# Kernel optimization log

Measured on AMD Instinct MI355X. Metric: run time of the kernel, lower is better.

Reference implementation:

```python
import math
import jax, jax.numpy as jnp
import numpy as np

GROUPS = 8
EPS = 1e-5


def setup_inputs() -> dict:
    key = jax.random.key(0)
    ks = jax.random.split(key, 4)
    B, C, H, W = 4, 128, 64, 64
    x = jax.random.normal(ks[0], (B, C, H, W), dtype=jnp.float32)
    norm_w = jnp.ones((C,), dtype=jnp.float32)
    norm_b = jnp.zeros((C,), dtype=jnp.float32)
    qkv_w = jax.random.normal(ks[1], (3 * C, C), dtype=jnp.float32) * 0.02
    qkv_b = jnp.zeros((3 * C,), dtype=jnp.float32)
    proj_w = jax.random.normal(ks[2], (C, C), dtype=jnp.float32) * 0.02
    proj_b = jnp.zeros((C,), dtype=jnp.float32)
    return {"x": x, "norm_w": norm_w, "norm_b": norm_b,
            "qkv_w": qkv_w, "qkv_b": qkv_b,
            "proj_w": proj_w, "proj_b": proj_b}


def reference(x, norm_w, norm_b, qkv_w, qkv_b, proj_w, proj_b):
    B, C, H, W = x.shape
    N = H * W
    # GroupNorm over (C/G, H, W) per group
    xr = x.reshape(B, GROUPS, C // GROUPS, N)
    mean = xr.mean(axis=(2, 3), keepdims=True)
    var = xr.var(axis=(2, 3), keepdims=True)
    h = ((xr - mean) * jax.lax.rsqrt(var + EPS)).reshape(B, C, N)
    h = h * norm_w[None, :, None] + norm_b[None, :, None]
    # 1x1 conv QKV == per-pixel linear: [B, 3C, N]
    qkv = jnp.einsum('oc,bcn->bon', qkv_w, h) + qkv_b[None, :, None]
    q, k, v = jnp.split(qkv, 3, axis=1)  # each [B, C, N]
    scale = 1.0 / math.sqrt(C)
    attn = jax.nn.softmax(jnp.einsum('bci,bcj->bij', q, k) * scale, axis=-1)  # [B,N,N]
    out = jnp.einsum('bij,bcj->bci', attn, v)  # [B, C, N]
    proj = jnp.einsum('oc,bcn->bon', proj_w, out) + proj_b[None, :, None]
    return x + proj.reshape(B, C, H, W)
```

## Files before the change

kernel.cpp:

```cpp
#include <hip/hip_runtime.h>

typedef float  f32x4   __attribute__((ext_vector_type(4)));
typedef float  f32x16  __attribute__((ext_vector_type(16)));
typedef short  bf16x8  __attribute__((ext_vector_type(8)));
typedef unsigned short u16;

constexpr int B_ = 4;
constexpr int C_ = 128;
constexpr int N_ = 4096;
constexpr int G_ = 8;
constexpr int CperG = 16;
constexpr float EPS_ = 1e-5f;
constexpr float SCALE_ = 0.08838834764831845f;

__device__ inline u16 f2bf(float f) {
    union { float f; unsigned u; } v; v.f = f;
    unsigned r = v.u + 0x7fffu + ((v.u >> 16) & 1u);
    return (u16)(r >> 16);
}
__device__ inline unsigned pk2(float a, float b) {
    return (unsigned)f2bf(a) | ((unsigned)f2bf(b) << 16);
}

__global__ __launch_bounds__(256) void prep_kernel(const float* __restrict__ x,
                                                   const float* __restrict__ qw,
                                                   const float* __restrict__ pw,
                                                   float* __restrict__ stats2,
                                                   u16* __restrict__ qwbf,
                                                   u16* __restrict__ pwbf) {
    int blk = blockIdx.x;
    if (blk < 256) {
        __shared__ float rs[4], rss[4];
        int bg = blk >> 3, chunk = blk & 7;
        const float4* xp = (const float4*)(x + (size_t)bg * (CperG * N_)) + chunk * 2048;
        float s = 0.f, ss = 0.f;
        for (int i = threadIdx.x; i < 2048; i += 256) {
            float4 v = xp[i];
            s  += v.x + v.y + v.z + v.w;
            ss += v.x*v.x + v.y*v.y + v.z*v.z + v.w*v.w;
        }
        #pragma unroll
        for (int off = 32; off > 0; off >>= 1) {
            s  += __shfl_down(s, off);
            ss += __shfl_down(ss, off);
        }
        int wv = threadIdx.x >> 6, ln = threadIdx.x & 63;
        if (ln == 0) { rs[wv] = s; rss[wv] = ss; }
        __syncthreads();
        if (threadIdx.x == 0) {
            stats2[blk*2]     = rs[0] + rs[1] + rs[2] + rs[3];
            stats2[blk*2 + 1] = rss[0] + rss[1] + rss[2] + rss[3];
        }
    } else {
        int fidx = ((blk - 256) * 256 + threadIdx.x) * 4;
        float4 v;
        u16* dst;
        if (fidx < 3*C_*C_) { v = *(const float4*)(qw + fidx); dst = qwbf + fidx; }
        else { int j = fidx - 3*C_*C_; v = *(const float4*)(pw + j); dst = pwbf + j; }
        ushort4 o;
        o.x = f2bf(v.x); o.y = f2bf(v.y); o.z = f2bf(v.z); o.w = f2bf(v.w);
        *(ushort4*)dst = o;
    }
}

constexpr int HS = 136;

__global__ __launch_bounds__(256, 2) void qkv_kernel(const float* __restrict__ x,
                                                     const float* __restrict__ stats2,
                                                     const float* __restrict__ nw,
                                                     const float* __restrict__ nb,
                                                     const u16* __restrict__ qwbf,
                                                     const float* __restrict__ qb,
                                                     u16* __restrict__ Qt,
                                                     u16* __restrict__ Ksw,
                                                     u16* __restrict__ Vsw,
                                                     float* __restrict__ qn2,
                                                     int* __restrict__ kmaxI) {
    int n0 = (blockIdx.x & 63) * 64;
    int b  = blockIdx.x >> 6;
    __shared__ u16 hs[64 * HS];
    __shared__ u16 Wl[64 * HS];
    __shared__ float gmean[8], grstd[8];
    int t = threadIdx.x;
    const float invM = 1.f / (float)(CperG * N_);
    if (t < 8) {
        const float* sp = stats2 + (size_t)(b*G_ + t)*16;
        float S = 0.f, SS = 0.f;
        #pragma unroll
        for (int k2 = 0; k2 < 8; ++k2) { S += sp[k2*2]; SS += sp[k2*2 + 1]; }
        float mean = S * invM;
        gmean[t] = mean;
        grstd[t] = rsqrtf(SS * invM - mean*mean + EPS_);
    }
    __syncthreads();
    #pragma unroll
    for (int r = 0; r < 8; ++r) {
        int idx = t + (r << 8);
        int c = idx >> 4, n4 = idx & 15;
        int g = c >> 4;
        float wgt = nw[c] * grstd[g];
        float bia = nb[c] - gmean[g] * wgt;
        float4 xv = *(const float4*)(x + ((size_t)(b*C_ + c))*N_ + n0 + n4*4);
        int base = (n4*4) * HS + c;
        hs[base         ] = f2bf(xv.x*wgt + bia);
        hs[base +     HS] = f2bf(xv.y*wgt + bia);
        hs[base + 2 * HS] = f2bf(xv.z*wgt + bia);
        hs[base + 3 * HS] = f2bf(xv.w*wgt + bia);
    }
    __syncthreads();
    int w = t >> 6, lane = t & 63, lo = lane & 15, hi = lane >> 4;
    bf16x8 hf[4];
    #pragma unroll
    for (int ch = 0; ch < 4; ++ch)
        hf[ch] = *(const bf16x8*)(hs + (16*w + lo)*HS + 32*ch + 8*hi);

    int Tb = (n0 >> 5) + (w >> 1);
    float nq = 0.f, nk = 0.f;
    for (int ck = 0; ck < 6; ++ck) {
        {
            int r = t >> 2, p = t & 3;
            const u16* src = qwbf + (size_t)(ck*64 + r)*C_ + p*32;
            u16* dst = Wl + r*HS + p*32;
            #pragma unroll
            for (int k2 = 0; k2 < 4; ++k2)
                *(uint4*)(dst + 8*k2) = *(const uint4*)(src + 8*k2);
        }
        __syncthreads();
        #pragma unroll
        for (int ot = 0; ot < 4; ++ot) {
            int o16 = ck*64 + ot*16;
            bf16x8 wf[4];
            #pragma unroll
            for (int ch = 0; ch < 4; ++ch)
                wf[ch] = *(const bf16x8*)(Wl + (ot*16 + lo)*HS + 32*ch + 8*hi);
            if (o16 < 2*C_) {
                f32x4 acc = (f32x4){0.f, 0.f, 0.f, 0.f};
                #pragma unroll
                for (int ch = 0; ch < 4; ++ch)
                    acc = __builtin_amdgcn_mfma_f32_16x16x32_bf16(wf[ch], hf[ch], acc, 0, 0, 0);
                float4 bv = *(const float4*)(qb + o16 + 4*hi);
                int n = n0 + 16*w + lo;
                ushort4 o4;
                if (o16 < C_) {
                    float q0 = (acc[0] + bv.x) * SCALE_;
                    float q1 = (acc[1] + bv.y) * SCALE_;
                    float q2 = (acc[2] + bv.z) * SCALE_;
                    float q3 = (acc[3] + bv.w) * SCALE_;
                    nq += (q0*q0 + q1*q1) + (q2*q2 + q3*q3);
                    o4.x = f2bf(q0); o4.y = f2bf(q1); o4.z = f2bf(q2); o4.w = f2bf(q3);
                    *(ushort4*)(Qt + ((size_t)b*N_ + n)*C_ + o16 + 4*hi) = o4;
                } else {
                    float k0 = acc[0] + bv.x, k1 = acc[1] + bv.y;
                    float k2 = acc[2] + bv.z, k3 = acc[3] + bv.w;
                    nk += (k0*k0 + k1*k1) + (k2*k2 + k3*k3);
                    o4.x = f2bf(k0); o4.y = f2bf(k1); o4.z = f2bf(k2); o4.w = f2bf(k3);
                    int cc = (o16 - C_) >> 4;
                    int lp = (16*(w & 1) + lo) + 32*(hi >> 1);
                    size_t fb = ((size_t)(b*128 + Tb)*8 + cc)*512;
                    *(ushort4*)(Ksw + fb + lp*8 + 4*(hi & 1)) = o4;
                }
            } else {
                f32x4 acc = (f32x4){0.f, 0.f, 0.f, 0.f};
                #pragma unroll
                for (int ch = 0; ch < 4; ++ch)
                    acc = __builtin_amdgcn_mfma_f32_16x16x32_bf16(hf[ch], wf[ch], acc, 0, 0, 0);
                float bia = qb[o16 + lo];
                ushort4 o4;
                o4.x = f2bf(acc[0] + bia);
                o4.y = f2bf(acc[1] + bia);
                o4.z = f2bf(acc[2] + bia);
                o4.w = f2bf(acc[3] + bia);
                int m  = (o16 - 2*C_) >> 4;
                int ct = m >> 1;
                int lp = (16*(m & 1) + lo) + 32*(hi & 1);
                size_t fb = (((size_t)(b*4 + ct)*128 + Tb)*2 + (w & 1))*512;
                *(ushort4*)(Vsw + fb + lp*8 + 4*(hi >> 1)) = o4;
            }
        }
        __syncthreads();
    }
    nq += __shfl_xor(nq, 16); nq += __shfl_xor(nq, 32);
    nk += __shfl_xor(nk, 16); nk += __shfl_xor(nk, 32);
    if (lane < 16) qn2[(size_t)b*N_ + n0 + 16*w + lo] = nq;
    #pragma unroll
    for (int off = 1; off < 16; off <<= 1)
        nk = fmaxf(nk, __shfl_xor(nk, off));
    if (lane == 0) atomicMax(&kmaxI[b], __float_as_int(nk));
}

__global__ __launch_bounds__(512, 2) void attn_kernel(const u16* __restrict__ Qt,
                                                      const u16* __restrict__ Ksw,
                                                      const u16* __restrict__ Vsw,
                                                      const float* __restrict__ qn2,
                                                      const int* __restrict__ kmaxI,
                                                      const u16* __restrict__ pwbf,
                                                      const float* __restrict__ pb,
                                                      const float* __restrict__ x,
                                                      float* __restrict__ out) {
    int lb = blockIdx.x;
    int b  = lb & 3;
    int i0 = 64 * (lb >> 2);
    int t = threadIdx.x;
    int w = t >> 6, lane = t & 63;
    int l31 = lane & 31, h = lane >> 5;
    int qt = w >> 2, ks = w & 3;

    __shared__ float Ob[64 * 132];
    __shared__ float lW[8][32];

    float kmax = sqrtf(__int_as_float(kmaxI[b]));
    float mq = sqrtf(qn2[(size_t)b*N_ + i0 + 32*qt + l31]) * kmax * 1.02f + 1e-6f;

    const u16* Qb = Qt + (size_t)b*N_*C_;
    bf16x8 qf[8];
    #pragma unroll
    for (int cc = 0; cc < 8; ++cc)
        qf[cc] = *(const bf16x8*)(Qb + (size_t)(i0 + 32*qt + l31)*C_ + 16*cc + 8*h);

    f32x16 acc[4];
    #pragma unroll
    for (int ct = 0; ct < 4; ++ct)
        #pragma unroll
        for (int r = 0; r < 16; ++r) acc[ct][r] = 0.f;
    float psum = 0.f;

    const u16* Kbase = Ksw + ((size_t)(b*128 + ks*32)*8)*512;
    bf16x8 kf[8], kn[8];
    #pragma unroll
    for (int cc = 0; cc < 8; ++cc)
        kf[cc] = *(const bf16x8*)(Kbase + cc*512 + lane*8);

    for (int it = 0; it < 32; ++it) {
        f32x16 s;
        #pragma unroll
        for (int r = 0; r < 16; ++r) s[r] = 0.f;
        #pragma unroll
        for (int cc = 0; cc < 8; ++cc)
            s = __builtin_amdgcn_mfma_f32_32x32x16_bf16(kf[cc], qf[cc], s, 0, 0, 0);
        {
            const u16* Kn = Kbase + ((size_t)(((it + 1) & 31))*8)*512;
            #pragma unroll
            for (int cc = 0; cc < 8; ++cc)
                kn[cc] = *(const bf16x8*)(Kn + cc*512 + lane*8);
        }
        int T = ks*32 + it;
        bf16x8 v1[4], v2[4];
        #pragma unroll
        for (int ct = 0; ct < 4; ++ct) {
            const u16* vb = Vsw + (((size_t)(b*4 + ct)*128 + T)*2)*512;
            v1[ct] = *(const bf16x8*)(vb + lane*8);
            v2[ct] = *(const bf16x8*)(vb + 512 + lane*8);
        }
        float p[16];
        #pragma unroll
        for (int r = 0; r < 16; ++r) {
            p[r] = __expf(s[r] - mq);
            psum += p[r];
        }
        union { bf16x8 v; unsigned u[4]; } pf1, pf2;
        pf1.u[0] = pk2(p[0],  p[1]);  pf1.u[1] = pk2(p[2],  p[3]);
        pf1.u[2] = pk2(p[4],  p[5]);  pf1.u[3] = pk2(p[6],  p[7]);
        pf2.u[0] = pk2(p[8],  p[9]);  pf2.u[1] = pk2(p[10], p[11]);
        pf2.u[2] = pk2(p[12], p[13]); pf2.u[3] = pk2(p[14], p[15]);
        #pragma unroll
        for (int ct = 0; ct < 4; ++ct) {
            acc[ct] = __builtin_amdgcn_mfma_f32_32x32x16_bf16(v1[ct], pf1.v, acc[ct], 0, 0, 0);
            acc[ct] = __builtin_amdgcn_mfma_f32_32x32x16_bf16(v2[ct], pf2.v, acc[ct], 0, 0, 0);
        }
        #pragma unroll
        for (int cc = 0; cc < 8; ++cc) kf[cc] = kn[cc];
    }

    psum += __shfl_xor(psum, 32);
    if (lane < 32) lW[w][l31] = psum;
    for (int i = 0; i < 4; ++i) {
        if (ks == i) {
            int q = 32*qt + l31;
            #pragma unroll
            for (int ct = 0; ct < 4; ++ct)
                #pragma unroll
                for (int qd = 0; qd < 4; ++qd) {
                    int c = 32*ct + 8*qd + 4*h;
                    float4 vv;
                    vv.x = acc[ct][4*qd + 0];
                    vv.y = acc[ct][4*qd + 1];
                    vv.z = acc[ct][4*qd + 2];
                    vv.w = acc[ct][4*qd + 3];
                    if (i == 0) {
                        *(float4*)(Ob + q*132 + c) = vv;
                    } else {
                        float4 o = *(const float4*)(Ob + q*132 + c);
                        o.x += vv.x; o.y += vv.y; o.z += vv.z; o.w += vv.w;
                        *(float4*)(Ob + q*132 + c) = o;
                    }
                }
        }
        __syncthreads();
    }
    int lo = lane & 15, hi = lane >> 4;
    int qtile = w >> 1, os = w & 1;
    int q = 16*qtile + lo;
    int qg = 4*(q >> 5), qc = q & 31;
    float linv = 1.f / (lW[qg][qc] + lW[qg+1][qc] + lW[qg+2][qc] + lW[qg+3][qc]);
    bf16x8 aa[4];
    #pragma unroll
    for (int ch = 0; ch < 4; ++ch) {
        float4 ua = *(const float4*)(Ob + q*132 + 32*ch + 8*hi);
        float4 ub = *(const float4*)(Ob + q*132 + 32*ch + 8*hi + 4);
        union { bf16x8 hh; unsigned u[4]; } pkd;
        pkd.u[0] = pk2(ua.x*linv, ua.y*linv);
        pkd.u[1] = pk2(ua.z*linv, ua.w*linv);
        pkd.u[2] = pk2(ub.x*linv, ub.y*linv);
        pkd.u[3] = pk2(ub.z*linv, ub.w*linv);
        aa[ch] = pkd.hh;
    }
    #pragma unroll
    for (int ot = 0; ot < 4; ++ot) {
        int ob = 64*os + 16*ot;
        f32x4 pr = (f32x4){0.f, 0.f, 0.f, 0.f};
        #pragma unroll
        for (int ch = 0; ch < 4; ++ch) {
            bf16x8 bw = *(const bf16x8*)(pwbf + (size_t)(ob + lo)*C_ + 32*ch + 8*hi);
            pr = __builtin_amdgcn_mfma_f32_16x16x32_bf16(aa[ch], bw, pr, 0, 0, 0);
        }
        int o = ob + lo;
        float pbv = pb[o];
        size_t base = ((size_t)(b*C_ + o))*N_ + i0 + 16*qtile + 4*hi;
        float4 xr = *(const float4*)(x + base);
        float4 res;
        res.x = xr.x + pr[0] + pbv;
        res.y = xr.y + pr[1] + pbv;
        res.z = xr.z + pr[2] + pbv;
        res.w = xr.w + pr[3] + pbv;
        *(float4*)(out + base) = res;
    }
}

extern "C" void kernel_launch(void* const* d_in, const int* in_sizes, int n_in,
                              void* d_out, int out_size, void* d_ws, size_t ws_size,
                              hipStream_t stream) {
    const float* x  = (const float*)d_in[0];
    const float* nw = (const float*)d_in[1];
    const float* nb = (const float*)d_in[2];
    const float* qw = (const float*)d_in[3];
    const float* qb = (const float*)d_in[4];
    const float* pw = (const float*)d_in[5];
    const float* pb = (const float*)d_in[6];
    float* out = (float*)d_out;

    char* p = (char*)d_ws;
    float* stats2 = (float*)p;                 p += 2048;
    float* qn2    = (float*)p;                 p += (size_t)B_*N_*4;
    int*   kmaxI  = (int*)p;                   p += 256;
    u16*   qwbf   = (u16*)p;                   p += (size_t)3*C_*C_*2;
    u16*   pwbf   = (u16*)p;                   p += (size_t)C_*C_*2;
    u16*   Qt     = (u16*)p;                   p += (size_t)B_*N_*C_*2;
    u16*   Ksw    = (u16*)p;                   p += (size_t)B_*N_*C_*2;
    u16*   Vsw    = (u16*)p;

    prep_kernel<<<dim3(320), 256, 0, stream>>>(x, qw, pw, stats2, qwbf, pwbf);
    qkv_kernel<<<dim3(256), 256, 0, stream>>>(x, stats2, nw, nb, qwbf, qb,
                                              Qt, Ksw, Vsw, qn2, kmaxI);
    attn_kernel<<<dim3(256), 512, 0, stream>>>(Qt, Ksw, Vsw, qn2, kmaxI,
                                               pwbf, pb, x, out);
}
```

Baseline: 152.8 us.

## Fuse prep, QKV and attention into one cooperative kernel with grid syncs

Replaces the three kernel launches with one cooperative kernel of 256 blocks by 512 threads. Phases are separated by grid.sync: stats and weight conversion first, then QKV projection, then attention. The QKV phase now uses 8 waves that split the output chunks across two wave groups, and norms are combined through shared memory. This removes launch gaps and inter-kernel drain, at the cost of grid-wide barriers, larger shared memory per block and lower occupancy in the QKV phase. The kmaxI reset is not visible in the shown code.

```diff
diff --git a/kernel.cpp b/kernel.cpp
--- a/kernel.cpp
+++ b/kernel.cpp
@@ -1,4 +1,7 @@
 #include <hip/hip_runtime.h>
+#include <hip/hip_cooperative_groups.h>
+
+namespace cg = cooperative_groups;
 
 typedef float  f32x4   __attribute__((ext_vector_type(4)));
 typedef float  f32x16  __attribute__((ext_vector_type(16)));
@@ -12,6 +15,7 @@
 constexpr int CperG = 16;
 constexpr float EPS_ = 1e-5f;
 constexpr float SCALE_ = 0.08838834764831845f;
+constexpr int HS = 136;
 
 __device__ inline u16 f2bf(float f) {
     union { float f; unsigned u; } v; v.f = f;
@@ -22,20 +26,43 @@
     return (unsigned)f2bf(a) | ((unsigned)f2bf(b) << 16);
 }
 
-__global__ __launch_bounds__(256) void prep_kernel(const float* __restrict__ x,
-                                                   const float* __restrict__ qw,
-                                                   const float* __restrict__ pw,
-                                                   float* __restrict__ stats2,
-                                                   u16* __restrict__ qwbf,
-                                                   u16* __restrict__ pwbf) {
+__global__ __launch_bounds__(512, 2) void fused_kernel(const float* __restrict__ x,
+                                                       const float* __restrict__ nw,
+                                                       const float* __restrict__ nb,
+                                                       const float* __restrict__ qw,
+                                                       const float* __restrict__ qb,
+                                                       const float* __restrict__ pw,
+                                                       const float* __restrict__ pb,
+                                                       float* __restrict__ stats2,
+                                                       float* __restrict__ qn2,
+                                                       int* __restrict__ kmaxI,
+                                                       u16* __restrict__ qwbf,
+                                                       u16* __restrict__ pwbf,
+                                                       u16* __restrict__ Qt,
+                                                       u16* __restrict__ Ksw,
+                                                       u16* __restrict__ Vsw,
+                                                       float* __restrict__ out) {
+    cg::grid_group grid = cg::this_grid();
+
+    __shared__ u16 hs[64 * HS];
+    __shared__ u16 Wl[128 * HS];
+    __shared__ float Ob[64 * 132];
+    __shared__ float lW[8][32];
+    __shared__ float rs[8], rss[8];
+    __shared__ float gmean[8], grstd[8];
+    __shared__ float nqS[2][64], nkS[2][64];
+
     int blk = blockIdx.x;
-    if (blk < 256) {
-        __shared__ float rs[4], rss[4];
+    int t = threadIdx.x;
+    int w = t >> 6, lane = t & 63, lo = lane & 15, hi = lane >> 4;
+
+    {
         int bg = blk >> 3, chunk = blk & 7;
         const float4* xp = (const float4*)(x + (size_t)bg * (CperG * N_)) + chunk * 2048;
         float s = 0.f, ss = 0.f;
-        for (int i = threadIdx.x; i < 2048; i += 256) {
-            float4 v = xp[i];
+        #pragma unroll
+        for (int r = 0; r < 4; ++r) {
+            float4 v = xp[t + (r << 9)];
             s  += v.x + v.y + v.z + v.w;
             ss += v.x*v.x + v.y*v.y + v.z*v.z + v.w*v.w;
         }
@@ -44,295 +71,280 @@
             s  += __shfl_down(s, off);
             ss += __shfl_down(ss, off);
         }
-        int wv = threadIdx.x >> 6, ln = threadIdx.x & 63;
-        if (ln == 0) { rs[wv] = s; rss[wv] = ss; }
-        __syncthreads();
-        if (threadIdx.x == 0) {
-            stats2[blk*2]     = rs[0] + rs[1] + rs[2] + rs[3];
-            stats2[blk*2 + 1] = rss[0] + rss[1] + rss[2] + rss[3];
-        }
-    } else {
-        int fidx = ((blk - 256) * 256 + threadIdx.x) * 4;
-        float4 v;
-        u16* dst;
-        if (fidx < 3*C_*C_) { v = *(const float4*)(qw + fidx); dst = qwbf + fidx; }
-        else { int j = fidx - 3*C_*C_; v = *(const float4*)(pw + j); dst = pwbf + j; }
-        ushort4 o;
-        o.x = f2bf(v.x); o.y = f2bf(v.y); o.z = f2bf(v.z); o.w = f2bf(v.w);
-        *(ushort4*)dst = o;
+        if (lane == 0) { rs[w] = s; rss[w] = ss; }
+        if (t < 64) {
+            int fidx = (blk*64 + t) * 4;
+            float4 v;
+            u16* dst;
+            if (fidx < 3*C_*C_) { v = *(const float4*)(qw + fidx); dst = qwbf + fidx; }
+            else { int j = fidx - 3*C_*C_; v = *(const float4*)(pw + j); dst = pwbf + j; }
+            ushort4 o;
+            o.x = f2bf(v.x); o.y = f2bf(v.y); o.z = f2bf(v.z); o.w = f2bf(v.w);
+            *(ushort4*)dst = o;
+        }
+        __syncthreads();
+        if (t == 0) {
+            float S = 0.f, SS = 0.f;
+            #pragma unroll
+            for (int i = 0; i < 8; ++i) { S += rs[i]; SS += rss[i]; }
+            stats2[blk*2]     = S;
+            stats2[blk*2 + 1] = SS;
+        }
     }
-}
-
-constexpr int HS = 136;
-
-__global__ __launch_bounds__(256, 2) void qkv_kernel(const float* __restrict__ x,
-                                                     const float* __restrict__ stats2,
-                                                     const float* __restrict__ nw,
-                                                     const float* __restrict__ nb,
-                                                     const u16* __restrict__ qwbf,
-                                                     const float* __restrict__ qb,
-                                                     u16* __restrict__ Qt,
-                                                     u16* __restrict__ Ksw,
-                                                     u16* __restrict__ Vsw,
-                                                     float* __restrict__ qn2,
-                                                     int* __restrict__ kmaxI) {
-    int n0 = (blockIdx.x & 63) * 64;
-    int b  = blockIdx.x >> 6;
-    __shared__ u16 hs[64 * HS];
-    __shared__ u16 Wl[64 * HS];
-    __shared__ float gmean[8], grstd[8];
-    int t = threadIdx.x;
-    const float invM = 1.f / (float)(CperG * N_);
-    if (t < 8) {
-        const float* sp = stats2 + (size_t)(b*G_ + t)*16;
-        float S = 0.f, SS = 0.f;
-        #pragma unroll
-        for (int k2 = 0; k2 < 8; ++k2) { S += sp[k2*2]; SS += sp[k2*2 + 1]; }
-        float mean = S * invM;
-        gmean[t] = mean;
-        grstd[t] = rsqrtf(SS * invM - mean*mean + EPS_);
-    }
-    __syncthreads();
-    #pragma unroll
-    for (int r = 0; r < 8; ++r) {
-        int idx = t + (r << 8);
-        int c = idx >> 4, n4 = idx & 15;
-        int g = c >> 4;
-        float wgt = nw[c] * grstd[g];
-        float bia = nb[c] - gmean[g] * wgt;
-        float4 xv = *(const float4*)(x + ((size_t)(b*C_ + c))*N_ + n0 + n4*4);
-        int base = (n4*4) * HS + c;
-        hs[base         ] = f2bf(xv.x*wgt + bia);
-        hs[base +     HS] = f2bf(xv.y*wgt + bia);
-        hs[base + 2 * HS] = f2bf(xv.z*wgt + bia);
-        hs[base + 3 * HS] = f2bf(xv.w*wgt + bia);
-    }
-    __syncthreads();
-    int w = t >> 6, lane = t & 63, lo = lane & 15, hi = lane >> 4;
-    bf16x8 hf[4];
-    #pragma unroll
-    for (int ch = 0; ch < 4; ++ch)
-        hf[ch] = *(const bf16x8*)(hs + (16*w + lo)*HS + 32*ch + 8*hi);
-
-    int Tb = (n0 >> 5) + (w >> 1);
-    float nq = 0.f, nk = 0.f;
-    for (int ck = 0; ck < 6; ++ck) {
-        {
-            int r = t >> 2, p = t & 3;
-            const u16* src = qwbf + (size_t)(ck*64 + r)*C_ + p*32;
-            u16* dst = Wl + r*HS + p*32;
-            #pragma unroll
-            for (int k2 = 0; k2 < 4; ++k2)
-                *(uint4*)(dst + 8*k2) = *(const uint4*)(src + 8*k2);
-        }
-        __syncthreads();
-        #pragma unroll
-        for (int ot = 0; ot < 4; ++ot) {
-            int o16 = ck*64 + ot*16;
-            bf16x8 wf[4];
-            #pragma unroll
-            for (int ch = 0; ch < 4; ++ch)
-                wf[ch] = *(const bf16x8*)(Wl + (ot*16 + lo)*HS + 32*ch + 8*hi);
-            if (o16 < 2*C_) {
-                f32x4 acc = (f32x4){0.f, 0.f, 0.f, 0.f};
+    __threadfence();
+    grid.sync();
+
+    {
+        int n0 = (blk & 63) * 64;
+        int b  = blk >> 6;
+        const float invM = 1.f / (float)(CperG * N_);
+        if (t < 8) {
+            const float* sp = stats2 + (size_t)(b*G_ + t)*16;
+            float S = 0.f, SS = 0.f;
+            #pragma unroll
+            for (int k2 = 0; k2 < 8; ++k2) { S += sp[k2*2]; SS += sp[k2*2 + 1]; }
+            float mean = S * invM;
+            gmean[t] = mean;
+            grstd[t] = rsqrtf(SS * invM - mean*mean + EPS_);
+        }
+        __syncthreads();
+        #pragma unroll
+        for (int r = 0; r < 4; ++r) {
+            int idx = t + (r << 9);
+            int c = idx >> 4, n4 = idx & 15;
+            int g = c >> 4;
+            float wgt = nw[c] * grstd[g];
+            float bia = nb[c] - gmean[g] * wgt;
+            float4 xv = *(const float4*)(x + ((size_t)(b*C_ + c))*N_ + n0 + n4*4);
+            int base = (n4*4) * HS + c;
+            hs[base         ] = f2bf(xv.x*wgt + bia);
+            hs[base +     HS] = f2bf(xv.y*wgt + bia);
+            hs[base + 2 * HS] = f2bf(xv.z*wgt + bia);
+            hs[base + 3 * HS] = f2bf(xv.w*wgt + bia);
+        }
+        __syncthreads();
+        int g2 = w >> 2;
+        int wl = w & 3;
+        bf16x8 hf[4];
+        #pragma unroll
+        for (int ch = 0; ch < 4; ++ch)
+            hf[ch] = *(const bf16x8*)(hs + (16*wl + lo)*HS + 32*ch + 8*hi);
+
+        int Tb = (n0 >> 5) + (wl >> 1);
+        float nq = 0.f, nk = 0.f;
+        for (int ck2 = 0; ck2 < 3; ++ck2) {
+            {
+                int r = t >> 2, p = t & 3;
+                const u16* src = qwbf + (size_t)(ck2*128 + r)*C_ + p*32;
+                u16* dst = Wl + r*HS + p*32;
+                #pragma unroll
+                for (int k2 = 0; k2 < 4; ++k2)
+                    *(uint4*)(dst + 8*k2) = *(const uint4*)(src + 8*k2);
+            }
+            __syncthreads();
+            int chunk = ck2*2 + g2;
+            #pragma unroll
+            for (int ot = 0; ot < 4; ++ot) {
+                int o16 = chunk*64 + ot*16;
+                bf16x8 wf[4];
                 #pragma unroll
                 for (int ch = 0; ch < 4; ++ch)
-                    acc = __builtin_amdgcn_mfma_f32_16x16x32_bf16(wf[ch], hf[ch], acc, 0, 0, 0);
-                float4 bv = *(const float4*)(qb + o16 + 4*hi);
-                int n = n0 + 16*w + lo;
-                ushort4 o4;
-                if (o16 < C_) {
-                    float q0 = (acc[0] + bv.x) * SCALE_;
-                    float q1 = (acc[1] + bv.y) * SCALE_;
-                    float q2 = (acc[2] + bv.z) * SCALE_;
-                    float q3 = (acc[3] + bv.w) * SCALE_;
-                    nq += (q0*q0 + q1*q1) + (q2*q2 + q3*q3);
-                    o4.x = f2bf(q0); o4.y = f2bf(q1); o4.z = f2bf(q2); o4.w = f2bf(q3);
-                    *(ushort4*)(Qt + ((size_t)b*N_ + n)*C_ + o16 + 4*hi) = o4;
+                    wf[ch] = *(const bf16x8*)(Wl + (64*g2 + ot*16 + lo)*HS + 32*ch + 8*hi);
+                if (o16 < 2*C_) {
+                    f32x4 acc = (f32x4){0.f, 0.f, 0.f, 0.f};
+                    #pragma unroll
+                    for (int ch = 0; ch < 4; ++ch)
+                        acc = __builtin_amdgcn_mfma_f32_16x16x32_bf16(wf[ch], hf[ch], acc, 0, 0, 0);
+                    float4 bv = *(const float4*)(qb + o16 + 4*hi);
+                    int n = n0 + 16*wl + lo;
+                    ushort4 o4;
+                    if (o16 < C_) {
+                        float q0 = (acc[0] + bv.x) * SCALE_;
+                        float q1 = (acc[1] + bv.y) * SCALE_;
+                        float q2 = (acc[2] + bv.z) * SCALE_;
+                        float q3 = (acc[3] + bv.w) * SCALE_;
+                        nq += (q0*q0 + q1*q1) + (q2*q2 + q3*q3);
+                        o4.x = f2bf(q0); o4.y = f2bf(q1); o4.z = f2bf(q2); o4.w = f2bf(q3);
+                        *(ushort4*)(Qt + ((size_t)b*N_ + n)*C_ + o16 + 4*hi) = o4;
+                    } else {
+                        float k0 = acc[0] + bv.x, k1 = acc[1] + bv.y;
+                        float k2 = acc[2] + bv.z, k3 = acc[3] + bv.w;
+                        nk += (k0*k0 + k1*k1) + (k2*k2 + k3*k3);
+                        o4.x = f2bf(k0); o4.y = f2bf(k1); o4.z = f2bf(k2); o4.w = f2bf(k3);
+                        int cc = (o16 - C_) >> 4;
+                        int lp = (16*(wl & 1) + lo) + 32*(hi >> 1);
+                        size_t fb = ((size_t)(b*128 + Tb)*8 + cc)*512;
+                        *(ushort4*)(Ksw + fb + lp*8 + 4*(hi & 1)) = o4;
+                    }
                 } else {
-                    float k0 = acc[0] + bv.x, k1 = acc[1] + bv.y;
-                    float k2 = acc[2] + bv.z, k3 = acc[3] + bv.w;
-                    nk += (k0*k0 + k1*k1) + (k2*k2 + k3*k3);
-                    o4.x = f2bf(k0); o4.y = f2bf(k1); o4.z = f2bf(k2); o4.w = f2bf(k3);
-                    int cc = (o16 - C_) >> 4;
-                    int lp = (16*(w & 1) + lo) + 32*(hi >> 1);
-                    size_t fb = ((size_t)(b*128 + Tb)*8 + cc)*512;
-                    *(ushort4*)(Ksw + fb + lp*8 + 4*(hi & 1)) = o4;
+                    f32x4 acc = (f32x4){0.f, 0.f, 0.f, 0.f};
+                    #pragma unroll
+                    for (int ch = 0; ch < 4; ++ch)
+                        acc = __builtin_amdgcn_mfma_f32_16x16x32_bf16(hf[ch], wf[ch], acc, 0, 0, 0);
+                    float bia = qb[o16 + lo];
+                    ushort4 o4;
+                    o4.x = f2bf(acc[0] + bia);
+                    o4.y = f2bf(acc[1] + bia);
+                    o4.z = f2bf(acc[2] + bia);
+                    o4.w = f2bf(acc[3] + bia);
+                    int m  = (o16 - 2*C_) >> 4;
+                    int ct = m >> 1;
+                    int lp = (16*(m & 1) + lo) + 32*(hi & 1);
+                    size_t fb = (((size_t)(b*4 + ct)*128 + Tb)*2 + (wl & 1))*512;
+                    *(ushort4*)(Vsw + fb + lp*8 + 4*(hi >> 1)) = o4;
                 }
-            } else {
-                f32x4 acc = (f32x4){0.f, 0.f, 0.f, 0.f};
+            }
+            __syncthreads();
+        }
+        nq += __shfl_xor(nq, 16); nq += __shfl_xor(nq, 32);
+        nk += __shfl_xor(nk, 16); nk += __shfl_xor(nk, 32);
+        if (lane < 16) { nqS[g2][16*wl + lo] = nq; nkS[g2][16*wl + lo] = nk; }
+        __syncthreads();
+        if (w < 4) {
+            float nqt = nqS[0][16*w + lo] + nqS[1][16*w + lo];
+            float nkt = nkS[0][16*w + lo] + nkS[1][16*w + lo];
+            if (lane < 16) qn2[(size_t)b*N_ + n0 + 16*w + lo] = nqt;
+            #pragma unroll
+            for (int off = 1; off < 16; off <<= 1)
+                nkt = fmaxf(nkt, __shfl_xor(nkt, off));
+            if (lane == 0) atomicMax(&kmaxI[b], __float_as_int(nkt));
+        }
+    }
+    __threadfence();
+    grid.sync();
+
+    {
+        int b  = blk & 3;
+        int i0 = 64 * (blk >> 2);
+        int l31 = lane & 31, h = lane >> 5;
+        int qt = w >> 2, ks = w & 3;
+
+        float kmax = sqrtf(__int_as_float(kmaxI[b]));
+        float mq = sqrtf(qn2[(size_t)b*N_ + i0 + 32*qt + l31]) * kmax * 1.02f + 1e-6f;
+
+        const u16* Qb = Qt + (size_t)b*N_*C_;
+        bf16x8 qf[8];
+        #pragma unroll
+        for (int cc = 0; cc < 8; ++cc)
+            qf[cc] = *(const bf16x8*)(Qb + (size_t)(i0 + 32*qt + l31)*C_ + 16*cc + 8*h);
+
+        f32x16 acc[4];
+        #pragma unroll
+        for (int ct = 0; ct < 4; ++ct)
+            #pragma unroll
+            for (int r = 0; r < 16; ++r) acc[ct][r] = 0.f;
+        float psum = 0.f;
+
+        const u16* Kbase = Ksw + ((size_t)(b*128 + ks*32)*8)*512;
+        bf16x8 kf[8], kn[8];
+        #pragma unroll
+        for (int cc = 0; cc < 8; ++cc)
+            kf[cc] = *(const bf16x8*)(Kbase + cc*512 + lane*8);
+
+        for (int it = 0; it < 32; ++it) {
+            f32x16 s;
+            #pragma unroll
+            for (int r = 0; r < 16; ++r) s[r] = 0.f;
+            #pragma unroll
+            for (int cc = 0; cc < 8; ++cc)
+                s = __builtin_amdgcn_mfma_f32_32x32x16_bf16(kf[cc], qf[cc], s, 0, 0, 0);
+            {
+                const u16* Kn = Kbase + ((size_t)(((it + 1) & 31))*8)*512;
                 #pragma unroll
-                for (int ch = 0; ch < 4; ++ch)
-                    acc = __builtin_amdgcn_mfma_f32_16x16x32_bf16(hf[ch], wf[ch], acc, 0, 0, 0);
-                float bia = qb[o16 + lo];
-                ushort4 o4;
-                o4.x = f2bf(acc[0] + bia);
-                o4.y = f2bf(acc[1] + bia);
-                o4.z = f2bf(acc[2] + bia);
-                o4.w = f2bf(acc[3] + bia);
-                int m  = (o16 - 2*C_) >> 4;
-                int ct = m >> 1;
-                int lp = (16*(m & 1) + lo) + 32*(hi & 1);
-                size_t fb = (((size_t)(b*4 + ct)*128 + Tb)*2 + (w & 1))*512;
-                *(ushort4*)(Vsw + fb + lp*8 + 4*(hi >> 1)) = o4;
-            }
-        }
-        __syncthreads();
-    }
-    nq += __shfl_xor(nq, 16); nq += __shfl_xor(nq, 32);
-    nk += __shfl_xor(nk, 16); nk += __shfl_xor(nk, 32);
-    if (lane < 16) qn2[(size_t)b*N_ + n0 + 16*w + lo] = nq;
-    #pragma unroll
-    for (int off = 1; off < 16; off <<= 1)
-        nk = fmaxf(nk, __shfl_xor(nk, off));
-    if (lane == 0) atomicMax(&kmaxI[b], __float_as_int(nk));
-}
-
-__global__ __launch_bounds__(512, 2) void attn_kernel(const u16* __restrict__ Qt,
-                                                      const u16* __restrict__ Ksw,
-                                                      const u16* __restrict__ Vsw,
-                                                      const float* __restrict__ qn2,
-                                                      const int* __restrict__ kmaxI,
-                                                      const u16* __restrict__ pwbf,
-                                                      const float* __restrict__ pb,
-                                                      const float* __restrict__ x,
-                                                      float* __restrict__ out) {
-    int lb = blockIdx.x;
-    int b  = lb & 3;
-    int i0 = 64 * (lb >> 2);
-    int t = threadIdx.x;
-    int w = t >> 6, lane = t & 63;
-    int l31 = lane & 31, h = lane >> 5;
-    int qt = w >> 2, ks = w & 3;
-
-    __shared__ float Ob[64 * 132];
-    __shared__ float lW[8][32];
-
-    float kmax = sqrtf(__int_as_float(kmaxI[b]));
-    float mq = sqrtf(qn2[(size_t)b*N_ + i0 + 32*qt + l31]) * kmax * 1.02f + 1e-6f;
-
-    const u16* Qb = Qt + (size_t)b*N_*C_;
-    bf16x8 qf[8];
-    #pragma unroll
-    for (int cc = 0; cc < 8; ++cc)
-        qf[cc] = *(const bf16x8*)(Qb + (size_t)(i0 + 32*qt + l31)*C_ + 16*cc + 8*h);
-
-    f32x16 acc[4];
-    #pragma unroll
-    for (int ct = 0; ct < 4; ++ct)
-        #pragma unroll
-        for (int r = 0; r < 16; ++r) acc[ct][r] = 0.f;
-    float psum = 0.f;
-
-    const u16* Kbase = Ksw + ((size_t)(b*128 + ks*32)*8)*512;
-    bf16x8 kf[8], kn[8];
-    #pragma unroll
-    for (int cc = 0; cc < 8; ++cc)
-        kf[cc] = *(const bf16x8*)(Kbase + cc*512 + lane*8);
-
-    for (int it = 0; it < 32; ++it) {
-        f32x16 s;
-        #pragma unroll
-        for (int r = 0; r < 16; ++r) s[r] = 0.f;
-        #pragma unroll
-        for (int cc = 0; cc < 8; ++cc)
-            s = __builtin_amdgcn_mfma_f32_32x32x16_bf16(kf[cc], qf[cc], s, 0, 0, 0);
-        {
-            const u16* Kn = Kbase + ((size_t)(((it + 1) & 31))*8)*512;
-            #pragma unroll
-            for (int cc = 0; cc < 8; ++cc)
-                kn[cc] = *(const bf16x8*)(Kn + cc*512 + lane*8);
-        }
-        int T = ks*32 + it;
-        bf16x8 v1[4], v2[4];
-        #pragma unroll
-        for (int ct = 0; ct < 4; ++ct) {
-            const u16* vb = Vsw + (((size_t)(b*4 + ct)*128 + T)*2)*512;
-            v1[ct] = *(const bf16x8*)(vb + lane*8);
-            v2[ct] = *(const bf16x8*)(vb + 512 + lane*8);
-        }
-        float p[16];
-        #pragma unroll
-        for (int r = 0; r < 16; ++r) {
-            p[r] = __expf(s[r] - mq);
-            psum += p[r];
-        }
-        union { bf16x8 v; unsigned u[4]; } pf1, pf2;
-        pf1.u[0] = pk2(p[0],  p[1]);  pf1.u[1] = pk2(p[2],  p[3]);
-        pf1.u[2] = pk2(p[4],  p[5]);  pf1.u[3] = pk2(p[6],  p[7]);
-        pf2.u[0] = pk2(p[8],  p[9]);  pf2.u[1] = pk2(p[10], p[11]);
-        pf2.u[2] = pk2(p[12], p[13]); pf2.u[3] = pk2(p[14], p[15]);
-        #pragma unroll
-        for (int ct = 0; ct < 4; ++ct) {
-            acc[ct] = __builtin_amdgcn_mfma_f32_32x32x16_bf16(v1[ct], pf1.v, acc[ct], 0, 0, 0);
-            acc[ct] = __builtin_amdgcn_mfma_f32_32x32x16_bf16(v2[ct], pf2.v, acc[ct], 0, 0, 0);
-        }
-        #pragma unroll
-        for (int cc = 0; cc < 8; ++cc) kf[cc] = kn[cc];
-    }
-
-    psum += __shfl_xor(psum, 32);
-    if (lane < 32) lW[w][l31] = psum;
-    for (int i = 0; i < 4; ++i) {
-        if (ks == i) {
-            int q = 32*qt + l31;
-            #pragma unroll
-            for (int ct = 0; ct < 4; ++ct)
+                for (int cc = 0; cc < 8; ++cc)
+                    kn[cc] = *(const bf16x8*)(Kn + cc*512 + lane*8);
+            }
+            int T = ks*32 + it;
+            bf16x8 v1[4], v2[4];
+            #pragma unroll
+            for (int ct = 0; ct < 4; ++ct) {
+                const u16* vb = Vsw + (((size_t)(b*4 + ct)*128 + T)*2)*512;
+                v1[ct] = *(const bf16x8*)(vb + lane*8);
+                v2[ct] = *(const bf16x8*)(vb + 512 + lane*8);
+            }
+            float p[16];
+            #pragma unroll
+            for (int r = 0; r < 16; ++r) {
+                p[r] = __expf(s[r] - mq);
+                psum += p[r];
+            }
+            union { bf16x8 v; unsigned u[4]; } pf1, pf2;
+            pf1.u[0] = pk2(p[0],  p[1]);  pf1.u[1] = pk2(p[2],  p[3]);
+            pf1.u[2] = pk2(p[4],  p[5]);  pf1.u[3] = pk2(p[6],  p[7]);
+            pf2.u[0] = pk2(p[8],  p[9]);  pf2.u[1] = pk2(p[10], p[11]);
+            pf2.u[2] = pk2(p[12], p[13]); pf2.u[3] = pk2(p[14], p[15]);
+            #pragma unroll
+            for (int ct = 0; ct < 4; ++ct) {
+                acc[ct] = __builtin_amdgcn_mfma_f32_32x32x16_bf16(v1[ct], pf1.v, acc[ct], 0, 0, 0);
+                acc[ct] = __builtin_amdgcn_mfma_f32_32x32x16_bf16(v2[ct], pf2.v, acc[ct], 0, 0, 0);
+            }
+            #pragma unroll
+            for (int cc = 0; cc < 8; ++cc) kf[cc] = kn[cc];
+        }
+
+        psum += __shfl_xor(psum, 32);
+        if (lane < 32) lW[w][l31] = psum;
+        __syncthreads();
+        for (int i = 0; i < 4; ++i) {
+            if (ks == i) {
+                int q = 32*qt + l31;
                 #pragma unroll
-                for (int qd = 0; qd < 4; ++qd) {
-                    int c = 32*ct + 8*qd + 4*h;
-                    float4 vv;
-                    vv.x = acc[ct][4*qd + 0];
-                    vv.y = acc[ct][4*qd + 1];
-                    vv.z = acc[ct][4*qd + 2];
-                    vv.w = acc[ct][4*qd + 3];
-                    if (i == 0) {
-                        *(float4*)(Ob + q*132 + c) = vv;
-                    } else {
-                        float4 o = *(const float4*)(Ob + q*132 + c);
-                        o.x += vv.x; o.y += vv.y; o.z += vv.z; o.w += vv.w;
-                        *(float4*)(Ob + q*132 + c) = o;
+                for (int ct = 0; ct < 4; ++ct)
+                    #pragma unroll
+                    for (int qd = 0; qd < 4; ++qd) {
+                        int c = 32*ct + 8*qd + 4*h;
+                        float4 vv;
+                        vv.x = acc[ct][4*qd + 0];
+                        vv.y = acc[ct][4*qd + 1];
+                        vv.z = acc[ct][4*qd + 2];
+                        vv.w = acc[ct][4*qd + 3];
+                        if (i == 0) {
+                            *(float4*)(Ob + q*132 + c) = vv;
+                        } else {
+                            float4 o = *(const float4*)(Ob + q*132 + c);
+                            o.x += vv.x; o.y += vv.y; o.z += vv.z; o.w += vv.w;
+                            *(float4*)(Ob + q*132 + c) = o;
+                        }
                     }
-                }
-        }
-        __syncthreads();
-    }
-    int lo = lane & 15, hi = lane >> 4;
-    int qtile = w >> 1, os = w & 1;
-    int q = 16*qtile + lo;
-    int qg = 4*(q >> 5), qc = q & 31;
-    float linv = 1.f / (lW[qg][qc] + lW[qg+1][qc] + lW[qg+2][qc] + lW[qg+3][qc]);
-    bf16x8 aa[4];
-    #pragma unroll
-    for (int ch = 0; ch < 4; ++ch) {
-        float4 ua = *(const float4*)(Ob + q*132 + 32*ch + 8*hi);
-        float4 ub = *(const float4*)(Ob + q*132 + 32*ch + 8*hi + 4);
-        union { bf16x8 hh; unsigned u[4]; } pkd;
-        pkd.u[0] = pk2(ua.x*linv, ua.y*linv);
-        pkd.u[1] = pk2(ua.z*linv, ua.w*linv);
-        pkd.u[2] = pk2(ub.x*linv, ub.y*linv);
-        pkd.u[3] = pk2(ub.z*linv, ub.w*linv);
-        aa[ch] = pkd.hh;
-    }
-    #pragma unroll
-    for (int ot = 0; ot < 4; ++ot) {
-        int ob = 64*os + 16*ot;
-        f32x4 pr = (f32x4){0.f, 0.f, 0.f, 0.f};
+            }
+            __syncthreads();
+        }
+        int qtile = w >> 1, os = w & 1;
+        int q = 16*qtile + lo;
+        int qg = 4*(q >> 5), qc = q & 31;
+        float linv = 1.f / (lW[qg][qc] + lW[qg+1][qc] + lW[qg+2][qc] + lW[qg+3][qc]);
+        bf16x8 aa[4];
         #pragma unroll
         for (int ch = 0; ch < 4; ++ch) {
-            bf16x8 bw = *(const bf16x8*)(pwbf + (size_t)(ob + lo)*C_ + 32*ch + 8*hi);
-            pr = __builtin_amdgcn_mfma_f32_16x16x32_bf16(aa[ch], bw, pr, 0, 0, 0);
-        }
-        int o = ob + lo;
-        float pbv = pb[o];
-        size_t base = ((size_t)(b*C_ + o))*N_ + i0 + 16*qtile + 4*hi;
-        float4 xr = *(const float4*)(x + base);
-        float4 res;
-        res.x = xr.x + pr[0] + pbv;
-        res.y = xr.y + pr[1] + pbv;
-        res.z = xr.z + pr[2] + pbv;
-        res.w = xr.w + pr[3] + pbv;
-        *(float4*)(out + base) = res;
+            float4 ua = *(const float4*)(Ob + q*132 + 32*ch + 8*hi);
+            float4 ub = *(const float4*)(Ob + q*132 + 32*ch + 8*hi + 4);
+            union { bf16x8 hh; unsigned u[4]; } pkd;
+            pkd.u[0] = pk2(ua.x*linv, ua.y*linv);
+            pkd.u[1] = pk2(ua.z*linv, ua.w*linv);
+            pkd.u[2] = pk2(ub.x*linv, ub.y*linv);
+            pkd.u[3] = pk2(ub.z*linv, ub.w*linv);
+            aa[ch] = pkd.hh;
+        }
+        #pragma unroll
+        for (int ot = 0; ot < 4; ++ot) {
+            int ob = 64*os + 16*ot;
+            f32x4 pr = (f32x4){0.f, 0.f, 0.f, 0.f};
+            #pragma unroll
+            for (int ch = 0; ch < 4; ++ch) {
+                bf16x8 bw = *(const bf16x8*)(pwbf + (size_t)(ob + lo)*C_ + 32*ch + 8*hi);
+                pr = __builtin_amdgcn_mfma_f32_16x16x32_bf16(aa[ch], bw, pr, 0, 0, 0);
+            }
+            int o = ob + lo;
+            float pbv = pb[o];
+            size_t base = ((size_t)(b*C_ + o))*N_ + i0 + 16*qtile + 4*hi;
+            float4 xr = *(const float4*)(x + base);
+            float4 res;
+            res.x = xr.x + pr[0] + pbv;
+            res.y = xr.y + pr[1] + pbv;
+            res.z = xr.z + pr[2] + pbv;
+            res.w = xr.w + pr[3] + pbv;
+            *(float4*)(out + base) = res;
+        }
     }
 }
 
@@ -358,9 +370,13 @@
     u16*   Ksw    = (u16*)p;                   p += (size_t)B_*N_*C_*2;
     u16*   Vsw    = (u16*)p;
 
-    prep_kernel<<<dim3(320), 256, 0, stream>>>(x, qw, pw, stats2, qwbf, pwbf);
-    qkv_kernel<<<dim3(256), 256, 0, stream>>>(x, stats2, nw, nb, qwbf, qb,
-                                              Qt, Ksw, Vsw, qn2, kmaxI);
-    attn_kernel<<<dim3(256), 512, 0, stream>>>(Qt, Ksw, Vsw, qn2, kmaxI,
-                                               pwbf, pb, x, out);
+    void* args[] = {
+        (void*)&x, (void*)&nw, (void*)&nb, (void*)&qw, (void*)&qb,
+        (void*)&pw, (void*)&pb,
+        (void*)&stats2, (void*)&qn2, (void*)&kmaxI,
+        (void*)&qwbf, (void*)&pwbf, (void*)&Qt, (void*)&Ksw, (void*)&Vsw,
+        (void*)&out
+    };
+    hipLaunchCooperativeKernel((void*)fused_kernel, dim3(256), dim3(512),
+                               args, 0, stream);
 }
```

Result: slower. 285.2 us (+86.6%).
